# Kernel optimization log

Hardware: AMD Instinct MI355X
Metric: run time of the kernel (lower is better)

The kernel has to match this reference:

```python
import jax, jax.numpy as jnp
import numpy as np

DIM = 512
HEADS = 8
HEAD_DIM = DIM // HEADS
SCALE = DIM ** (-0.5)  # source uses full dim, not head_dim
LAMBDA_COND = 1.0


def setup_inputs() -> dict:
    key = jax.random.key(0)
    ks = jax.random.split(key, 16)
    b, n, m_a, m_s = 4, 2048, 2048, 256
    s = 0.02
    inp = {
        "x": jax.random.normal(ks[0], (b, n, DIM), jnp.float32),
        "audio_context": jax.random.normal(ks[1], (b, m_a, DIM), jnp.float32),
        "singer_context": jax.random.normal(ks[2], (b, m_s, DIM), jnp.float32),
        "Wq": jax.random.normal(ks[3], (DIM, DIM), jnp.float32) * s,
        "bq": jnp.zeros((DIM,), jnp.float32),
        "Wka": jax.random.normal(ks[4], (DIM, DIM), jnp.float32) * s,
        "bka": jnp.zeros((DIM,), jnp.float32),
        "Wva": jax.random.normal(ks[5], (DIM, DIM), jnp.float32) * s,
        "bva": jnp.zeros((DIM,), jnp.float32),
        "Wks": jax.random.normal(ks[6], (DIM, DIM), jnp.float32) * s,
        "bks": jnp.zeros((DIM,), jnp.float32),
        "Wvs": jax.random.normal(ks[7], (DIM, DIM), jnp.float32) * s,
        "bvs": jnp.zeros((DIM,), jnp.float32),
        "Wp": jax.random.normal(ks[8], (DIM, DIM), jnp.float32) * s,
        "bp": jnp.zeros((DIM,), jnp.float32),
    }
    return inp


def _heads(t):
    b, n, c = t.shape
    return t.reshape(b, n, HEADS, HEAD_DIM).transpose(0, 2, 1, 3)  # (b,h,n,d)


def _attend(q, ctx, Wk, bk, Wv, bv):
    k = _heads(ctx @ Wk.T + bk)
    v = _heads(ctx @ Wv.T + bv)
    attn = jax.nn.softmax(jnp.einsum("bhnd,bhmd->bhnm", q, k) * SCALE, axis=-1)
    o = jnp.einsum("bhnm,bhmd->bhnd", attn, v)
    b, h, n, d = o.shape
    return o.transpose(0, 2, 1, 3).reshape(b, n, h * d)


def reference(x, audio_context, singer_context, Wq, bq, Wka, bka, Wva, bva,
              Wks, bks, Wvs, bvs, Wp, bp):
    q = _heads(x @ Wq.T + bq)
    x_audio = _attend(q, audio_context, Wka, bka, Wva, bva)
    x_singer = _attend(q, singer_context, Wks, bks, Wvs, bvs)
    out = x_audio + LAMBDA_COND * x_singer
    return out @ Wp.T + bp
```

## Files before the change

kernel.cpp:

```cpp
#include <hip/hip_runtime.h>

#define DIM 512
#define NQ 2048
#define MA 2048
#define MS 256
#define QSCALE 0.06375864651f

typedef __attribute__((ext_vector_type(8))) short bf16x8;
typedef __attribute__((ext_vector_type(4))) float f32x4;
typedef __attribute__((ext_vector_type(16))) float f32x16;

__device__ __forceinline__ ushort f2b(float f) {
    uint u = __float_as_uint(f);
    u = (u + 0x7fffu + ((u >> 16) & 1u)) >> 16;
    return (ushort)u;
}

__device__ __forceinline__ uint pk2bf(float a, float b) {
#if __has_builtin(__builtin_amdgcn_cvt_pk_bf16_f32)
    typedef __attribute__((ext_vector_type(2))) __bf16 bf2;
    bf2 r = __builtin_amdgcn_cvt_pk_bf16_f32(a, b);
    uint u;
    __builtin_memcpy(&u, &r, 4);
    return u;
#else
    return ((__float_as_uint(a) + 0x8000u) >> 16) |
           ((__float_as_uint(b) + 0x8000u) & 0xffff0000u);
#endif
}

__device__ __forceinline__ float fexp2(float x) {
#if __has_builtin(__builtin_amdgcn_exp2f)
    return __builtin_amdgcn_exp2f(x);
#else
    return exp2f(x);
#endif
}

__device__ __forceinline__ void gload16(const ushort* g, ushort* l) {
    __builtin_amdgcn_global_load_lds(
        (const __attribute__((address_space(1))) void*)g,
        (__attribute__((address_space(3))) void*)l, 16, 0, 0);
}

__global__ __launch_bounds__(256) void cast_all(const float* __restrict__ w0,
                                                const float* __restrict__ w1,
                                                const float* __restrict__ w2,
                                                const float* __restrict__ w3,
                                                const float* __restrict__ w4,
                                                const float* __restrict__ w5,
                                                const float* __restrict__ x,
                                                const float* __restrict__ ac,
                                                const float* __restrict__ scx,
                                                ushort* __restrict__ dst) {
    int i = blockIdx.x * 256 + threadIdx.x;
    const float* s;
    int o;
    if (i < 393216) {
        int w = i >> 16;
        s = w < 3 ? (w == 0 ? w0 : (w == 1 ? w1 : w2))
                  : (w == 3 ? w3 : (w == 4 ? w4 : w5));
        o = i & 65535;
    } else if (i < 1441792) { s = x;   o = i - 393216; }
    else if (i < 2490368)   { s = ac;  o = i - 1441792; }
    else                    { s = scx; o = i - 2490368; }
    float4 v = ((const float4*)s)[o];
    ushort4 u;
    u.x = f2b(v.x); u.y = f2b(v.y); u.z = f2b(v.z); u.w = f2b(v.w);
    ((ushort4*)dst)[i] = u;
}

struct GD {
    const ushort* A; const ushort* B; const float* bias; void* out;
    long sB, sO;
    int N, bx, by, blk0, biasrow, scaleq, outf32, pad;
};

__global__ __launch_bounds__(256) void gemm_fused(GD d0, GD d1, GD d2, GD d3, GD d4) {
    __shared__ ushort At[128 * 32];
    __shared__ ushort Bt[128 * 32];
    GD d = d0;
    int bid = blockIdx.x;
    if (bid >= d1.blk0) d = d1;
    if (bid >= d2.blk0) d = d2;
    if (bid >= d3.blk0) d = d3;
    if (bid >= d4.blk0) d = d4;
    int local = bid - d.blk0;
    int x = local % d.bx;
    int rem = local / d.bx;
    int y = rem % d.by;
    int z = rem / d.by;

    int t = threadIdx.x;
    int wv = t >> 6, ln = t & 63, l = ln & 15, g = ln >> 4;
    int wrow = wv & 1, wcol = wv >> 1;
    int row0 = x * 128, col0 = y * 128;
    int srow = t >> 2;
    int slot = (t & 3) * 8;
    int sko = ((t ^ srow) & 3) * 8;
    int kc8 = ((g ^ (l & 3)) & 3) * 8;
    const ushort* Ab = d.A;
    const ushort* Bb = d.B + (size_t)z * d.sB;
    int N = d.N;

    f32x4 acc[4][4];
#pragma unroll
    for (int i = 0; i < 4; i++)
#pragma unroll
        for (int j = 0; j < 4; j++) acc[i][j] = (f32x4){0, 0, 0, 0};

    for (int k0 = 0; k0 < 512; k0 += 32) {
        __syncthreads();
#pragma unroll
        for (int c = 0; c < 2; c++) {
            gload16(Ab + (size_t)(row0 + srow + 64 * c) * 512 + k0 + sko,
                    At + (srow + 64 * c) * 32 + slot);
            gload16(Bb + (size_t)(col0 + srow + 64 * c) * 512 + k0 + sko,
                    Bt + (srow + 64 * c) * 32 + slot);
        }
        __syncthreads();
        bf16x8 ar[4], br[4];
#pragma unroll
        for (int i = 0; i < 4; i++)
            ar[i] = *(const bf16x8*)(At + (wrow * 64 + i * 16 + l) * 32 + kc8);
#pragma unroll
        for (int j = 0; j < 4; j++)
            br[j] = *(const bf16x8*)(Bt + (wcol * 64 + j * 16 + l) * 32 + kc8);
#pragma unroll
        for (int i = 0; i < 4; i++)
#pragma unroll
            for (int j = 0; j < 4; j++)
                acc[i][j] = __builtin_amdgcn_mfma_f32_16x16x32_bf16(ar[i], br[j], acc[i][j], 0, 0, 0);
    }
#pragma unroll
    for (int i = 0; i < 4; i++) {
#pragma unroll
        for (int j = 0; j < 4; j++) {
            int row = row0 + wrow * 64 + i * 16 + g * 4;
            int col = col0 + wcol * 64 + j * 16 + l;
#pragma unroll
            for (int r = 0; r < 4; r++) {
                float bv = d.biasrow ? d.bias[row + r] : d.bias[col];
                float o = acc[i][j][r] + bv;
                if (d.scaleq) o *= QSCALE;
                if (d.outf32)
                    ((float*)d.out + (size_t)z * d.sO)[(size_t)(row + r) * N + col] = o;
                else
                    ((ushort*)d.out + (size_t)z * d.sO)[(size_t)(row + r) * N + col] = f2b(o);
            }
        }
    }
}

__device__ __forceinline__ void attn_ctx32(const ushort* __restrict__ kg,
                                           const ushort* __restrict__ vg,
                                           int M, const bf16x8 (&aq)[4],
                                           ushort* __restrict__ Kl,
                                           ushort* __restrict__ Vl,
                                           f32x16 (&o)[2], float& li,
                                           int l5, int hi, int sr, int sc, int vbase) {
    int nt = M >> 6;
    bf16x8 k0 = *(const bf16x8*)kg;
    bf16x8 k1 = *(const bf16x8*)(kg + (size_t)32 * DIM);
    bf16x8 v0 = *(const bf16x8*)vg;
    bf16x8 v1 = *(const bf16x8*)(vg + (size_t)32 * M);
    __syncthreads();
    {
        *(bf16x8*)(Kl + sr * 72 + sc) = k0;
        *(bf16x8*)(Kl + (sr + 32) * 72 + sc) = k1;
        union { bf16x8 v; uint2 h[2]; } cv;
        cv.v = v0;
        *(uint2*)(Vl + sr * 72 + vbase) = cv.h[0];
        *(uint2*)(Vl + sr * 72 + vbase + 8) = cv.h[1];
        cv.v = v1;
        *(uint2*)(Vl + (sr + 32) * 72 + vbase) = cv.h[0];
        *(uint2*)(Vl + (sr + 32) * 72 + vbase + 8) = cv.h[1];
    }
    if (nt > 1) {
        k0 = *(const bf16x8*)(kg + (size_t)64 * DIM);
        k1 = *(const bf16x8*)(kg + (size_t)96 * DIM);
        v0 = *(const bf16x8*)(vg + 64);
        v1 = *(const bf16x8*)(vg + (size_t)32 * M + 64);
    }
    for (int i = 0; i < nt; i++) {
        __syncthreads();
        if (i + 1 < nt) {
            ushort* Kb = Kl + ((i + 1) & 1) * (64 * 72);
            ushort* Vb = Vl + ((i + 1) & 1) * (64 * 72);
            *(bf16x8*)(Kb + sr * 72 + sc) = k0;
            *(bf16x8*)(Kb + (sr + 32) * 72 + sc) = k1;
            union { bf16x8 v; uint2 h[2]; } cv;
            cv.v = v0;
            *(uint2*)(Vb + sr * 72 + vbase) = cv.h[0];
            *(uint2*)(Vb + sr * 72 + vbase + 8) = cv.h[1];
            cv.v = v1;
            *(uint2*)(Vb + (sr + 32) * 72 + vbase) = cv.h[0];
            *(uint2*)(Vb + (sr + 32) * 72 + vbase + 8) = cv.h[1];
        }
        if (i + 2 < nt) {
            size_t off = (size_t)(i + 2) * 64;
            k0 = *(const bf16x8*)(kg + off * DIM);
            k1 = *(const bf16x8*)(kg + (off + 32) * DIM);
            v0 = *(const bf16x8*)(vg + off);
            v1 = *(const bf16x8*)(vg + (size_t)32 * M + off);
        }
        const ushort* Kc = Kl + (i & 1) * (64 * 72);
        const ushort* Vc = Vl + (i & 1) * (64 * 72);
        uint2 pq[2][4];
#pragma unroll
        for (int c = 0; c < 2; c++) {
            bf16x8 kf[4];
#pragma unroll
            for (int kd = 0; kd < 4; kd++)
                kf[kd] = *(const bf16x8*)(Kc + (32 * c + l5) * 72 + kd * 16 + hi * 8);
            f32x16 s;
#pragma unroll
            for (int ii = 0; ii < 16; ii++) s[ii] = 0.f;
#pragma unroll
            for (int kd = 0; kd < 4; kd++)
                s = __builtin_amdgcn_mfma_f32_32x32x16_bf16(kf[kd], aq[kd], s, 0, 0, 0);
#pragma unroll
            for (int m = 0; m < 4; m++) {
                float p0 = fexp2(s[4 * m + 0]);
                float p1 = fexp2(s[4 * m + 1]);
                float p2 = fexp2(s[4 * m + 2]);
                float p3 = fexp2(s[4 * m + 3]);
                li += (p0 + p1) + (p2 + p3);
                pq[c][m].x = pk2bf(p0, p1);
                pq[c][m].y = pk2bf(p2, p3);
            }
        }
#pragma unroll
        for (int kc = 0; kc < 4; kc++) {
            int c = kc >> 1, m0 = 2 * (kc & 1);
            union { bf16x8 v; uint u[4]; } w;
            w.u[0] = pq[c][m0].x;     w.u[1] = pq[c][m0].y;
            w.u[2] = pq[c][m0 + 1].x; w.u[3] = pq[c][m0 + 1].y;
#pragma unroll
            for (int dn = 0; dn < 2; dn++) {
                bf16x8 vf = *(const bf16x8*)(Vc + (32 * dn + l5) * 72 + kc * 16 + hi * 8);
                o[dn] = __builtin_amdgcn_mfma_f32_32x32x16_bf16(w.v, vf, o[dn], 0, 0, 0);
            }
        }
    }
}

__global__ __launch_bounds__(256) void attn_kernel(const ushort* __restrict__ q,
                                                   const ushort* __restrict__ Ka,
                                                   const ushort* __restrict__ VTa,
                                                   const ushort* __restrict__ Ks,
                                                   const ushort* __restrict__ VTs,
                                                   ushort* __restrict__ y) {
    __shared__ ushort Kl[2 * 64 * 72];
    __shared__ ushort Vl[2 * 64 * 72];
    int t = threadIdx.x;
    int wv = t >> 6, ln = t & 63, l5 = ln & 31, hi = ln >> 5;
    int h = blockIdx.y, bi = blockIdx.z;
    int q0 = blockIdx.x * 128 + wv * 32;
    bf16x8 aq[4];
    const ushort* qp = q + (size_t)(bi * NQ + q0 + l5) * DIM + h * 64 + hi * 8;
#pragma unroll
    for (int kd = 0; kd < 4; kd++) aq[kd] = *(const bf16x8*)(qp + kd * 16);
    int sr = t >> 3, sc = (t & 7) * 8;
    int vbase = (sc >> 4) * 16 + ((sc >> 3) & 1) * 4;

    f32x16 o[2];
#pragma unroll
    for (int dn = 0; dn < 2; dn++)
#pragma unroll
        for (int i = 0; i < 16; i++) o[dn][i] = 0.f;
    float li = 0.f;

    attn_ctx32(Ks + (size_t)bi * MS * DIM + (size_t)sr * DIM + h * 64 + sc,
               VTs + (size_t)bi * DIM * MS + (size_t)(h * 64 + sr) * MS + sc,
               MS, aq, Kl, Vl, o, li, l5, hi, sr, sc, vbase);
    li += __shfl_xor(li, 32);
    float inv[16];
#pragma unroll
    for (int rg = 0; rg < 16; rg++)
        inv[rg] = 1.f / __shfl(li, (rg & 3) + 8 * (rg >> 2) + 4 * hi);
    float yv[2][16];
#pragma unroll
    for (int dn = 0; dn < 2; dn++)
#pragma unroll
        for (int rg = 0; rg < 16; rg++) yv[dn][rg] = o[dn][rg] * inv[rg];

#pragma unroll
    for (int dn = 0; dn < 2; dn++)
#pragma unroll
        for (int i = 0; i < 16; i++) o[dn][i] = 0.f;
    li = 0.f;
    attn_ctx32(Ka + (size_t)bi * MA * DIM + (size_t)sr * DIM + h * 64 + sc,
               VTa + (size_t)bi * DIM * MA + (size_t)(h * 64 + sr) * MA + sc,
               MA, aq, Kl, Vl, o, li, l5, hi, sr, sc, vbase);
    li += __shfl_xor(li, 32);
#pragma unroll
    for (int rg = 0; rg < 16; rg++)
        inv[rg] = 1.f / __shfl(li, (rg & 3) + 8 * (rg >> 2) + 4 * hi);

#pragma unroll
    for (int dn = 0; dn < 2; dn++)
#pragma unroll
        for (int rg = 0; rg < 16; rg++) {
            int qr = (rg & 3) + 8 * (rg >> 2) + 4 * hi;
            float ov = yv[dn][rg] + o[dn][rg] * inv[rg];
            y[(size_t)(bi * NQ + q0 + qr) * DIM + h * 64 + 32 * dn + l5] = f2b(ov);
        }
}

extern "C" void kernel_launch(void* const* d_in, const int* in_sizes, int n_in,
                              void* d_out, int out_size, void* d_ws, size_t ws_size,
                              hipStream_t stream) {
    const float* x   = (const float*)d_in[0];
    const float* ac  = (const float*)d_in[1];
    const float* scx = (const float*)d_in[2];
    const float* Wq  = (const float*)d_in[3];
    const float* bq  = (const float*)d_in[4];
    const float* Wka = (const float*)d_in[5];
    const float* bka = (const float*)d_in[6];
    const float* Wva = (const float*)d_in[7];
    const float* bva = (const float*)d_in[8];
    const float* Wks = (const float*)d_in[9];
    const float* bks = (const float*)d_in[10];
    const float* Wvs = (const float*)d_in[11];
    const float* bvs = (const float*)d_in[12];
    const float* Wp  = (const float*)d_in[13];
    const float* bp  = (const float*)d_in[14];

    ushort* wb   = (ushort*)d_ws;
    ushort* wqb  = wb;
    ushort* wkab = wb + 262144;
    ushort* wvab = wb + 2 * 262144;
    ushort* wksb = wb + 3 * 262144;
    ushort* wvsb = wb + 4 * 262144;
    ushort* wpb  = wb + 5 * 262144;
    ushort* xb   = wb + 6 * 262144;
    ushort* acb  = xb + 4194304;
    ushort* scxb = acb + 4194304;
    ushort* qb   = scxb + 524288;
    ushort* kab  = qb + 4194304;
    ushort* vta  = kab + 4194304;
    ushort* ksb  = vta + 4194304;
    ushort* vts  = ksb + 524288;
    ushort* yb   = xb;

    cast_all<<<10240, 256, 0, stream>>>(Wq, Wka, Wva, Wks, Wvs, Wp, x, ac, scx, wb);

    GD gq   = {xb,   wqb,  bq,  qb,  0, 0,               512,  64, 4,  0,   0, 1, 0, 0};
    GD gka  = {acb,  wkab, bka, kab, 0, 0,               512,  64, 4,  256, 0, 0, 0, 0};
    GD gvta = {wvab, acb,  bva, vta, 2048L * 512, 512L * 2048, 2048, 4, 16, 512, 1, 0, 0, 0};
    GD gks  = {scxb, wksb, bks, ksb, 0, 0,               512,  8,  4,  768, 0, 0, 0, 0};
    GD gvts = {wvsb, scxb, bvs, vts, 256L * 512, 512L * 256,   256,  4,  2,  800, 1, 0, 0, 0};
    gemm_fused<<<832, 256, 0, stream>>>(gq, gka, gvta, gks, gvts);

    attn_kernel<<<dim3(16, 8, 4), 256, 0, stream>>>(qb, kab, vta, ksb, vts, yb);

    GD gpr = {yb, wpb, bp, d_out, 0, 0, 512, 64, 4, 0, 0, 0, 1, 0};
    GD gnv = {nullptr, nullptr, nullptr, nullptr, 0, 0, 0, 1, 1, 1 << 30, 0, 0, 0, 0};
    gemm_fused<<<256, 256, 0, stream>>>(gpr, gnv, gnv, gnv, gnv);
}
```

Measured before the change: 228.3 us.

## Split attention context across two wave groups per block and merge partials

Doubles the attention block to 512 threads, with two groups of four waves that each process half of the key/value context (split-K style) for the same 128 queries. Partial outputs and row sums from the second group go through shared memory and are added into the first group before normalization. The grid is only 512 blocks, so this aims to raise wave occupancy on the many-CU GPU and shorten each block's serial loop over keys. The cost is extra barriers, an LDS reduction, and higher register pressure under launch_bounds(512,4). Both groups skip the running max in the same way, so summing raw partials is consistent with the existing softmax.

Measured after the change: 227.9 us. No clear change (-0.2%).

```diff
diff --git a/kernel.cpp b/kernel.cpp
--- a/kernel.cpp
+++ b/kernel.cpp
@@ -154,12 +154,11 @@
 
 __device__ __forceinline__ void attn_ctx32(const ushort* __restrict__ kg,
                                            const ushort* __restrict__ vg,
-                                           int M, const bf16x8 (&aq)[4],
+                                           int M, int nt, const bf16x8 (&aq)[4],
                                            ushort* __restrict__ Kl,
                                            ushort* __restrict__ Vl,
                                            f32x16 (&o)[2], float& li,
                                            int l5, int hi, int sr, int sc, int vbase) {
-    int nt = M >> 6;
     bf16x8 k0 = *(const bf16x8*)kg;
     bf16x8 k1 = *(const bf16x8*)(kg + (size_t)32 * DIM);
     bf16x8 v0 = *(const bf16x8*)vg;
@@ -245,23 +244,28 @@
     }
 }
 
-__global__ __launch_bounds__(256) void attn_kernel(const ushort* __restrict__ q,
-                                                   const ushort* __restrict__ Ka,
-                                                   const ushort* __restrict__ VTa,
-                                                   const ushort* __restrict__ Ks,
-                                                   const ushort* __restrict__ VTs,
-                                                   ushort* __restrict__ y) {
-    __shared__ ushort Kl[2 * 64 * 72];
-    __shared__ ushort Vl[2 * 64 * 72];
+__global__ __launch_bounds__(512, 4) void attn_kernel(const ushort* __restrict__ q,
+                                                      const ushort* __restrict__ Ka,
+                                                      const ushort* __restrict__ VTa,
+                                                      const ushort* __restrict__ Ks,
+                                                      const ushort* __restrict__ VTs,
+                                                      ushort* __restrict__ y) {
+    __shared__ ushort smem[2 * 18432];
     int t = threadIdx.x;
-    int wv = t >> 6, ln = t & 63, l5 = ln & 31, hi = ln >> 5;
+    int grp = t >> 8;
+    int tg = t & 255;
+    int wg = tg >> 6;
+    int ln = t & 63, l5 = ln & 31, hi = ln >> 5;
+    ushort* Kl = smem + grp * 18432;
+    ushort* Vl = Kl + 9216;
+    float* osc = (float*)(smem + 18432);
     int h = blockIdx.y, bi = blockIdx.z;
-    int q0 = blockIdx.x * 128 + wv * 32;
+    int q0 = blockIdx.x * 128 + wg * 32;
     bf16x8 aq[4];
     const ushort* qp = q + (size_t)(bi * NQ + q0 + l5) * DIM + h * 64 + hi * 8;
 #pragma unroll
     for (int kd = 0; kd < 4; kd++) aq[kd] = *(const bf16x8*)(qp + kd * 16);
-    int sr = t >> 3, sc = (t & 7) * 8;
+    int sr = tg >> 3, sc = (tg & 7) * 8;
     int vbase = (sc >> 4) * 16 + ((sc >> 3) & 1) * 4;
 
     f32x16 o[2];
@@ -271,41 +275,79 @@
         for (int i = 0; i < 16; i++) o[dn][i] = 0.f;
     float li = 0.f;
 
-    attn_ctx32(Ks + (size_t)bi * MS * DIM + (size_t)sr * DIM + h * 64 + sc,
-               VTs + (size_t)bi * DIM * MS + (size_t)(h * 64 + sr) * MS + sc,
-               MS, aq, Kl, Vl, o, li, l5, hi, sr, sc, vbase);
+    attn_ctx32(Ks + (size_t)bi * MS * DIM + (size_t)(grp * 128 + sr) * DIM + h * 64 + sc,
+               VTs + (size_t)bi * DIM * MS + (size_t)(h * 64 + sr) * MS + grp * 128 + sc,
+               MS, 2, aq, Kl, Vl, o, li, l5, hi, sr, sc, vbase);
     li += __shfl_xor(li, 32);
-    float inv[16];
-#pragma unroll
-    for (int rg = 0; rg < 16; rg++)
-        inv[rg] = 1.f / __shfl(li, (rg & 3) + 8 * (rg >> 2) + 4 * hi);
+    __syncthreads();
+    if (grp) {
+        float* p = osc + (wg * 64 + ln) * 34;
+#pragma unroll
+        for (int dn = 0; dn < 2; dn++)
+#pragma unroll
+            for (int k = 0; k < 8; k++)
+                *(float2*)(p + dn * 16 + 2 * k) = (float2){o[dn][2 * k], o[dn][2 * k + 1]};
+        p[32] = li;
+    }
+    __syncthreads();
     float yv[2][16];
-#pragma unroll
-    for (int dn = 0; dn < 2; dn++)
-#pragma unroll
-        for (int rg = 0; rg < 16; rg++) yv[dn][rg] = o[dn][rg] * inv[rg];
+    if (!grp) {
+        const float* p = osc + (wg * 64 + ln) * 34;
+#pragma unroll
+        for (int dn = 0; dn < 2; dn++)
+#pragma unroll
+            for (int k = 0; k < 16; k++) o[dn][k] += p[dn * 16 + k];
+        li += p[32];
+        float inv[16];
+#pragma unroll
+        for (int rg = 0; rg < 16; rg++)
+            inv[rg] = 1.f / __shfl(li, (rg & 3) + 8 * (rg >> 2) + 4 * hi);
+#pragma unroll
+        for (int dn = 0; dn < 2; dn++)
+#pragma unroll
+            for (int rg = 0; rg < 16; rg++) yv[dn][rg] = o[dn][rg] * inv[rg];
+    }
 
 #pragma unroll
     for (int dn = 0; dn < 2; dn++)
 #pragma unroll
         for (int i = 0; i < 16; i++) o[dn][i] = 0.f;
     li = 0.f;
-    attn_ctx32(Ka + (size_t)bi * MA * DIM + (size_t)sr * DIM + h * 64 + sc,
-               VTa + (size_t)bi * DIM * MA + (size_t)(h * 64 + sr) * MA + sc,
-               MA, aq, Kl, Vl, o, li, l5, hi, sr, sc, vbase);
+    attn_ctx32(Ka + (size_t)bi * MA * DIM + (size_t)(grp * 1024 + sr) * DIM + h * 64 + sc,
+               VTa + (size_t)bi * DIM * MA + (size_t)(h * 64 + sr) * MA + grp * 1024 + sc,
+               MA, 16, aq, Kl, Vl, o, li, l5, hi, sr, sc, vbase);
     li += __shfl_xor(li, 32);
-#pragma unroll
-    for (int rg = 0; rg < 16; rg++)
-        inv[rg] = 1.f / __shfl(li, (rg & 3) + 8 * (rg >> 2) + 4 * hi);
-
-#pragma unroll
-    for (int dn = 0; dn < 2; dn++)
-#pragma unroll
-        for (int rg = 0; rg < 16; rg++) {
-            int qr = (rg & 3) + 8 * (rg >> 2) + 4 * hi;
-            float ov = yv[dn][rg] + o[dn][rg] * inv[rg];
-            y[(size_t)(bi * NQ + q0 + qr) * DIM + h * 64 + 32 * dn + l5] = f2b(ov);
-        }
+    __syncthreads();
+    if (grp) {
+        float* p = osc + (wg * 64 + ln) * 34;
+#pragma unroll
+        for (int dn = 0; dn < 2; dn++)
+#pragma unroll
+            for (int k = 0; k < 8; k++)
+                *(float2*)(p + dn * 16 + 2 * k) = (float2){o[dn][2 * k], o[dn][2 * k + 1]};
+        p[32] = li;
+    }
+    __syncthreads();
+    if (!grp) {
+        const float* p = osc + (wg * 64 + ln) * 34;
+#pragma unroll
+        for (int dn = 0; dn < 2; dn++)
+#pragma unroll
+            for (int k = 0; k < 16; k++) o[dn][k] += p[dn * 16 + k];
+        li += p[32];
+        float inv[16];
+#pragma unroll
+        for (int rg = 0; rg < 16; rg++)
+            inv[rg] = 1.f / __shfl(li, (rg & 3) + 8 * (rg >> 2) + 4 * hi);
+#pragma unroll
+        for (int dn = 0; dn < 2; dn++)
+#pragma unroll
+            for (int rg = 0; rg < 16; rg++) {
+                int qr = (rg & 3) + 8 * (rg >> 2) + 4 * hi;
+                float ov = yv[dn][rg] + o[dn][rg] * inv[rg];
+                y[(size_t)(bi * NQ + q0 + qr) * DIM + h * 64 + 32 * dn + l5] = f2b(ov);
+            }
+    }
 }
 
 extern "C" void kernel_launch(void* const* d_in, const int* in_sizes, int n_in,
@@ -353,7 +395,7 @@
     GD gvts = {wvsb, scxb, bvs, vts, 256L * 512, 512L * 256,   256,  4,  2,  800, 1, 0, 0, 0};
     gemm_fused<<<832, 256, 0, stream>>>(gq, gka, gvta, gks, gvts);
 
-    attn_kernel<<<dim3(16, 8, 4), 256, 0, stream>>>(qb, kab, vta, ksb, vts, yb);
+    attn_kernel<<<dim3(16, 8, 4), 512, 0, stream>>>(qb, kab, vta, ksb, vts, yb);
 
     GD gpr = {yb, wpb, bp, d_out, 0, 0, 512, 64, 4, 0, 0, 0, 1, 0};
     GD gnv = {nullptr, nullptr, nullptr, nullptr, 0, 0, 0, 1, 1, 1 << 30, 0, 0, 0, 0};
```
